# Performance work log

Measured on AMD Instinct MI355X. Metric: run time of the kernel, lower is better.

## Reference

```python
import jax, jax.numpy as jnp
import numpy as np

N_BINS = 15


def setup_inputs() -> dict:
    key = jax.random.key(0)
    k1, k2 = jax.random.split(key)
    N, C = 2097152, 50
    logits = jax.random.normal(k1, (N, C), dtype=jnp.float32)
    labels = jax.random.randint(k2, (N,), 0, C, dtype=jnp.int64)
    return {"logits": logits, "labels": labels}


def reference(logits, labels):
    n = logits.shape[0]
    probs = jax.nn.softmax(logits, axis=1)
    confidences = jnp.max(probs, axis=1)                 # [N]
    predictions = jnp.argmax(probs, axis=1)              # [N]
    accuracies = (predictions == labels).astype(jnp.float32)

    # bin i covers (i/n_bins, (i+1)/n_bins]; searchsorted(left) on the upper
    # boundaries gives the first upper >= conf, matching conf.gt(lo)*conf.le(hi)
    uppers = jnp.linspace(0.0, 1.0, N_BINS + 1)[1:]
    bin_id = jnp.clip(jnp.searchsorted(uppers, confidences, side="left"), 0, N_BINS - 1)

    ones = jnp.ones_like(confidences)
    counts = jax.ops.segment_sum(ones, bin_id, num_segments=N_BINS)
    sum_acc = jax.ops.segment_sum(accuracies, bin_id, num_segments=N_BINS)
    sum_conf = jax.ops.segment_sum(confidences, bin_id, num_segments=N_BINS)

    prop_in_bin = counts / n
    nonempty = counts > 0
    denom = jnp.maximum(counts, 1.0)
    avg_acc = sum_acc / denom
    avg_conf = sum_conf / denom

    gap = avg_conf - avg_acc
    bin_over_confidence = jnp.where(nonempty, gap * prop_in_bin, 0.0)   # [n_bins]
    ece = jnp.sum(jnp.where(nonempty, jnp.abs(gap) * prop_in_bin, 0.0)).reshape(1)
    return (ece, bin_over_confidence, prop_in_bin)
```

## Files before the change

### kernel.cpp

```cpp
#include <hip/hip_runtime.h>
#include <math.h>

#define N_BINS 15
#define C 50
#define ROWS_PER_TILE 64
#define TILE_FLOATS (ROWS_PER_TILE * C)
#define WAVES_PER_BLOCK 4
#define BLOCK (WAVES_PER_BLOCK * 64)
#define GRID 768


__device__ __forceinline__ void load_lds16(const float* g, float* l) {
    __builtin_amdgcn_global_load_lds(
        (const __attribute__((address_space(1))) unsigned int*)g,
        (__attribute__((address_space(3))) unsigned int*)l, 16, 0, 0);
}

__global__ __launch_bounds__(BLOCK) void ece_accum(
    const float* __restrict__ logits,
    const int*   __restrict__ labels,
    unsigned int* __restrict__ ws_cnt,
    unsigned int* __restrict__ ws_acc,
    float*        __restrict__ ws_conf,
    int n_rows)
{
    __shared__ float tiles[WAVES_PER_BLOCK * TILE_FLOATS];
    __shared__ unsigned int s_cnt[N_BINS];
    __shared__ unsigned int s_acc[N_BINS];
    __shared__ float        s_conf[N_BINS];

    const int tid = threadIdx.x;
    if (tid < N_BINS) { s_cnt[tid] = 0u; s_acc[tid] = 0u; s_conf[tid] = 0.0f; }
    __syncthreads();

    const int wave = tid >> 6;
    const int lane = tid & 63;
    float* __restrict__ wtile = &tiles[wave * TILE_FLOATS];

    const int n_tiles  = n_rows / ROWS_PER_TILE;
    const int gwave    = blockIdx.x * WAVES_PER_BLOCK + wave;
    const int n_gwaves = GRID * WAVES_PER_BLOCK;

    for (int t = gwave; t < n_tiles; t += n_gwaves) {
        const float* __restrict__ src = logits + (size_t)t * TILE_FLOATS;

        asm volatile("s_waitcnt lgkmcnt(0)" ::: "memory");

        #pragma unroll
        for (int j = 0; j < 12; ++j)
            load_lds16(src + (j * 64 + lane) * 4, wtile + j * 256);
        if (lane < 32)
            load_lds16(src + (12 * 64 + lane) * 4, wtile + 12 * 256);

        int label = labels[t * ROWS_PER_TILE + lane];

        asm volatile("s_waitcnt vmcnt(0)" ::: "memory");

        const float2* __restrict__ r2 = (const float2*)(wtile + lane * C);
        float vals[C];
        #pragma unroll
        for (int k = 0; k < C / 2; ++k) {
            float2 p = r2[k];
            vals[2 * k]     = p.x;
            vals[2 * k + 1] = p.y;
        }

        float vmax = vals[0];
        int   amax = 0;
        #pragma unroll
        for (int k = 1; k < C; ++k)
            if (vals[k] > vmax) { vmax = vals[k]; amax = k; }

        float sum = 0.0f;
        #pragma unroll
        for (int k = 0; k < C; ++k) sum += __expf(vals[k] - vmax);
        float conf = 1.0f / sum;

        int bin = (int)ceilf(conf * 15.0f) - 1;
        bin = bin < 0 ? 0 : (bin > N_BINS - 1 ? N_BINS - 1 : bin);

        atomicAdd(&s_cnt[bin], 1u);
        if (amax == label) atomicAdd(&s_acc[bin], 1u);
        atomicAdd(&s_conf[bin], conf);
    }

    const int rem_start = n_tiles * ROWS_PER_TILE;
    const int rem = n_rows - rem_start;
    if (blockIdx.x == 0 && tid < rem) {
        const float* __restrict__ r = logits + (size_t)(rem_start + tid) * C;
        float vmax = r[0];
        int   amax = 0;
        for (int k = 1; k < C; ++k) {
            float v = r[k];
            if (v > vmax) { vmax = v; amax = k; }
        }
        float sum = 0.0f;
        for (int k = 0; k < C; ++k) sum += __expf(r[k] - vmax);
        float conf = 1.0f / sum;
        int bin = (int)ceilf(conf * 15.0f) - 1;
        bin = bin < 0 ? 0 : (bin > N_BINS - 1 ? N_BINS - 1 : bin);
        atomicAdd(&s_cnt[bin], 1u);
        if (amax == labels[rem_start + tid]) atomicAdd(&s_acc[bin], 1u);
        atomicAdd(&s_conf[bin], conf);
    }

    __syncthreads();
    if (tid < N_BINS && s_cnt[tid] != 0u) {
        atomicAdd(&ws_cnt[tid],  s_cnt[tid]);
        atomicAdd(&ws_acc[tid],  s_acc[tid]);
        atomicAdd(&ws_conf[tid], s_conf[tid]);
    }
}

__global__ __launch_bounds__(64) void ece_final(
    const unsigned int* __restrict__ ws_cnt,
    const unsigned int* __restrict__ ws_acc,
    const float*        __restrict__ ws_conf,
    float* __restrict__ out, float inv_n)
{
    int i = threadIdx.x;
    float v = 0.0f;
    if (i < N_BINS) {
        float cnt      = (float)ws_cnt[i];
        float prop     = cnt * inv_n;
        float denom    = fmaxf(cnt, 1.0f);
        float avg_acc  = (float)ws_acc[i] / denom;
        float avg_conf = ws_conf[i] / denom;
        float gap      = avg_conf - avg_acc;
        bool  nonempty = cnt > 0.0f;
        out[1 + i]  = nonempty ? gap * prop : 0.0f;
        out[16 + i] = prop;
        v = nonempty ? fabsf(gap) * prop : 0.0f;
    }
    v += __shfl_down(v, 8, 64);
    v += __shfl_down(v, 4, 64);
    v += __shfl_down(v, 2, 64);
    v += __shfl_down(v, 1, 64);
    if (i == 0) out[0] = v;
}

extern "C" void kernel_launch(void* const* d_in, const int* in_sizes, int n_in,
                              void* d_out, int out_size, void* d_ws, size_t ws_size,
                              hipStream_t stream)
{
    const float* logits = (const float*)d_in[0];
    const int*   labels = (const int*)d_in[1];
    const int n_rows = in_sizes[1];

    unsigned int* ws_cnt  = (unsigned int*)d_ws;
    unsigned int* ws_acc  = ws_cnt + N_BINS;
    float*        ws_conf = (float*)(ws_acc + N_BINS);

    hipMemsetAsync(d_ws, 0, 3 * N_BINS * sizeof(float), stream);

    ece_accum<<<GRID, BLOCK, 0, stream>>>(logits, labels, ws_cnt, ws_acc, ws_conf, n_rows);
    ece_final<<<1, 64, 0, stream>>>(ws_cnt, ws_acc, ws_conf, (float*)d_out,
                                    1.0f / (float)n_rows);
}
```

Baseline: 553.3 us.

## Double-buffer per-wave LDS tiles and stage labels through LDS

Each wave now owns two LDS buffers and prefetches the next tile, including its labels via global_load_lds, while it computes on the current tile. The wait uses a partial vmcnt so only the current tile's loads must finish. Waves per block drop from 4 to 2 to fit the doubled LDS footprint, which trades occupancy for memory-level overlap. The hard-coded vmcnt(14) relies on exact per-lane load counts, and lanes issuing fewer loads may not be covered correctly.

```diff
diff --git a/kernel.cpp b/kernel.cpp
--- a/kernel.cpp
+++ b/kernel.cpp
@@ -3,10 +3,11 @@
 
 #define N_BINS 15
 #define C 50
-#define ROWS_PER_TILE 64
-#define TILE_FLOATS (ROWS_PER_TILE * C)
-#define WAVES_PER_BLOCK 4
-#define BLOCK (WAVES_PER_BLOCK * 64)
+#define ROWS 64
+#define TILE_LOG 3200
+#define TILE_FLOATS 3264
+#define WPB 2
+#define BLOCK (WPB * 64)
 #define GRID 768
 
 
@@ -14,6 +15,16 @@
     __builtin_amdgcn_global_load_lds(
         (const __attribute__((address_space(1))) unsigned int*)g,
         (__attribute__((address_space(3))) unsigned int*)l, 16, 0, 0);
+}
+
+__device__ __forceinline__ void stage_tile(const float* __restrict__ src,
+                                           const int* __restrict__ lbl,
+                                           float* __restrict__ dst, int lane) {
+    #pragma unroll
+    for (int j = 0; j < 12; ++j)
+        load_lds16(src + (j * 64 + lane) * 4, dst + j * 256);
+    if (lane < 32) load_lds16(src + (12 * 64 + lane) * 4, dst + 12 * 256);
+    if (lane < 16) load_lds16((const float*)lbl + lane * 4, dst + TILE_LOG);
 }
 
 __global__ __launch_bounds__(BLOCK) void ece_accum(
@@ -24,7 +35,7 @@
     float*        __restrict__ ws_conf,
     int n_rows)
 {
-    __shared__ float tiles[WAVES_PER_BLOCK * TILE_FLOATS];
+    __shared__ float tiles[WPB * 2 * TILE_FLOATS];
     __shared__ unsigned int s_cnt[N_BINS];
     __shared__ unsigned int s_acc[N_BINS];
     __shared__ float        s_conf[N_BINS];
@@ -35,28 +46,32 @@
 
     const int wave = tid >> 6;
     const int lane = tid & 63;
-    float* __restrict__ wtile = &tiles[wave * TILE_FLOATS];
+    float* __restrict__ buf0 = &tiles[(wave * 2 + 0) * TILE_FLOATS];
+    float* __restrict__ buf1 = &tiles[(wave * 2 + 1) * TILE_FLOATS];
 
-    const int n_tiles  = n_rows / ROWS_PER_TILE;
-    const int gwave    = blockIdx.x * WAVES_PER_BLOCK + wave;
-    const int n_gwaves = GRID * WAVES_PER_BLOCK;
+    const int n_tiles  = n_rows / ROWS;
+    const int gwave    = blockIdx.x * WPB + wave;
+    const int n_gwaves = GRID * WPB;
 
-    for (int t = gwave; t < n_tiles; t += n_gwaves) {
-        const float* __restrict__ src = logits + (size_t)t * TILE_FLOATS;
+    int t = gwave;
+    int cur = 0;
+    if (t < n_tiles)
+        stage_tile(logits + (size_t)t * TILE_LOG, labels + t * ROWS, buf0, lane);
 
-        asm volatile("s_waitcnt lgkmcnt(0)" ::: "memory");
+    for (; t < n_tiles; t += n_gwaves) {
+        const int tn = t + n_gwaves;
+        const bool has_next = tn < n_tiles;
+        float* __restrict__ bufc = cur ? buf1 : buf0;
+        float* __restrict__ bufn = cur ? buf0 : buf1;
 
-        #pragma unroll
-        for (int j = 0; j < 12; ++j)
-            load_lds16(src + (j * 64 + lane) * 4, wtile + j * 256);
-        if (lane < 32)
-            load_lds16(src + (12 * 64 + lane) * 4, wtile + 12 * 256);
+        if (has_next) {
+            stage_tile(logits + (size_t)tn * TILE_LOG, labels + tn * ROWS, bufn, lane);
+            asm volatile("s_waitcnt vmcnt(14)" ::: "memory");
+        } else {
+            asm volatile("s_waitcnt vmcnt(0)" ::: "memory");
+        }
 
-        int label = labels[t * ROWS_PER_TILE + lane];
-
-        asm volatile("s_waitcnt vmcnt(0)" ::: "memory");
-
-        const float2* __restrict__ r2 = (const float2*)(wtile + lane * C);
+        const float2* __restrict__ r2 = (const float2*)(bufc + lane * C);
         float vals[C];
         #pragma unroll
         for (int k = 0; k < C / 2; ++k) {
@@ -64,6 +79,7 @@
             vals[2 * k]     = p.x;
             vals[2 * k + 1] = p.y;
         }
+        const int label = ((const int*)bufc)[TILE_LOG + lane];
 
         float vmax = vals[0];
         int   amax = 0;
@@ -82,9 +98,11 @@
         atomicAdd(&s_cnt[bin], 1u);
         if (amax == label) atomicAdd(&s_acc[bin], 1u);
         atomicAdd(&s_conf[bin], conf);
+
+        cur ^= 1;
     }
 
-    const int rem_start = n_tiles * ROWS_PER_TILE;
+    const int rem_start = n_tiles * ROWS;
     const int rem = n_rows - rem_start;
     if (blockIdx.x == 0 && tid < rem) {
         const float* __restrict__ r = logits + (size_t)(rem_start + tid) * C;
```

Measured after the change: 556.6 us. About the same (+0.6%).
